# Kernel tuning notes

Hardware: AMD Instinct MI355X
Metric: run time of the kernel (lower is better)

## Reference

```python
import jax, jax.numpy as jnp
import numpy as np

B, T, D = 4, 1024, 1024       # batch, tokens, emb_size
E, K, F_EXP = 8, 2, 1024      # num_expert, num_expert_active, expert_size
NUM_BLOCK = 12


def setup_inputs() -> dict:
    key = jax.random.key(0)
    k_x, k_b, k_r, k_1, k_2 = jax.random.split(key, 5)
    x = jax.random.normal(k_x, (B, T, D), dtype=jnp.float32)
    auxfree_bias = jax.random.normal(k_b, (E,), dtype=jnp.float32) * 0.1
    router_w = jax.random.normal(k_r, (E, D), dtype=jnp.float32) * 0.02
    # GroupedLinear weight{i}: [out_features, in_features], applied as x @ W^T
    w1 = jax.random.normal(k_1, (E, F_EXP, D), dtype=jnp.float32) * 0.02
    w2 = jax.random.normal(k_2, (E, D, F_EXP), dtype=jnp.float32) * (0.02 / np.sqrt(2.0 * NUM_BLOCK))
    return {"x": x, "auxfree_bias": auxfree_bias, "router_w": router_w, "w1": w1, "w2": w2}


def reference(x, auxfree_bias, router_w, w1, w2):
    # --- routing: top-k on bias-adjusted DETACHED logits, gather raw logits ---
    logits = jnp.einsum("btd,ed->bte", x, router_w)              # [B,T,E]
    biased = jax.lax.stop_gradient(logits) + auxfree_bias        # bias only affects selection
    _, idx = jax.lax.top_k(biased, K)                            # [B,T,K] int32
    gathered = jnp.take_along_axis(logits, idx, axis=-1)         # [B,T,K]
    probs = jax.nn.softmax(gathered, axis=-1)                    # [B,T,K]

    # combine weights per expert: sum_k probs_k * 1[idx_k == e]  -> [B,T,E]
    combine = jnp.sum(jax.nn.one_hot(idx, E, dtype=x.dtype) * probs[..., None], axis=2)

    # --- experts: out = sum_e combine_e * (gelu(x W1_e^T) W2_e^T) ---
    # (dense per-expert reference for the dispatch -> grouped GEMM -> combine pipeline;
    #  tokens with combine weight 0 contribute nothing, matching the sparse original)
    out = jnp.zeros_like(x)
    for e in range(E):
        h = jax.nn.gelu(jnp.einsum("btd,fd->btf", x, w1[e]), approximate=False)
        out = out + combine[:, :, e:e + 1] * jnp.einsum("btf,df->btd", h, w2[e])
    return out
```

## Files before the change

kernel.cpp:

```cpp
#include <hip/hip_runtime.h>
#include <hip/hip_bf16.h>

#define D_DIM 1024
#define F_DIM 1024
#define NTOK  4096
#define NEXP  8
#define CAP   4096

typedef __attribute__((ext_vector_type(8))) short bf16x8;
typedef __attribute__((ext_vector_type(4))) float f32x4;
typedef __attribute__((ext_vector_type(8))) unsigned short u16x8;

__device__ __forceinline__ unsigned short f2bf(float f) {
    unsigned int u = __float_as_uint(f);
    u = u + 0x7fffu + ((u >> 16) & 1u);
    return (unsigned short)(u >> 16);
}

__device__ __forceinline__ void async_copy16(void* lds, const void* gsrc) {
    __builtin_amdgcn_global_load_lds(
        (const __attribute__((address_space(1))) unsigned int*)gsrc,
        (__attribute__((address_space(3))) unsigned int*)lds, 16, 0, 0);
}

__global__ __launch_bounds__(256) void cvt_kernel(const float* __restrict__ in,
                                                  unsigned short* __restrict__ out, int n) {
    int i = (blockIdx.x * 256 + threadIdx.x) * 8;
    if (i >= n) return;
    const float4* p = (const float4*)(in + i);
    float4 a = p[0], b = p[1];
    u16x8 r;
    r[0] = f2bf(a.x); r[1] = f2bf(a.y); r[2] = f2bf(a.z); r[3] = f2bf(a.w);
    r[4] = f2bf(b.x); r[5] = f2bf(b.y); r[6] = f2bf(b.z); r[7] = f2bf(b.w);
    *(u16x8*)(out + i) = r;
}

__global__ __launch_bounds__(256) void logits_kernel(
    const float* __restrict__ x, const float* __restrict__ rw,
    float* __restrict__ logits)
{
    const int wave = threadIdx.x >> 6, lane = threadIdx.x & 63;
    const int t = blockIdx.x * 4 + wave;
    double s[NEXP];
    #pragma unroll
    for (int e = 0; e < NEXP; ++e) s[e] = 0.0;
    const float* xp = x + (size_t)t * D_DIM;
    for (int kk = 0; kk < D_DIM; kk += 64) {
        float xv = xp[kk + lane];
        #pragma unroll
        for (int e = 0; e < NEXP; ++e)
            s[e] += (double)xv * (double)rw[e * D_DIM + kk + lane];
    }
    #pragma unroll
    for (int e = 0; e < NEXP; ++e) {
        double v = s[e];
        for (int off = 32; off; off >>= 1) v += __shfl_xor(v, off, 64);
        s[e] = v;
    }
    if (lane == 0) {
        #pragma unroll
        for (int e = 0; e < NEXP; ++e) logits[(size_t)t * NEXP + e] = (float)s[e];
    }
}

__global__ __launch_bounds__(256) void assign_kernel(
    const float* __restrict__ logits, const float* __restrict__ bias,
    int* counts, int* list, float* wlist)
{
    __shared__ int lcnt[NEXP];
    __shared__ int lbase[NEXP];
    const int tid = threadIdx.x;
    const int t = blockIdx.x * 256 + tid;
    if (tid < NEXP) lcnt[tid] = 0;
    __syncthreads();

    float lg[NEXP], b2[NEXP];
    #pragma unroll
    for (int e = 0; e < NEXP; ++e) {
        lg[e] = logits[(size_t)t * NEXP + e];
        b2[e] = lg[e] + bias[e];
    }
    int i0 = 0; float b0v = b2[0], l0v = lg[0];
    #pragma unroll
    for (int e = 1; e < NEXP; ++e)
        if (b2[e] > b0v) { b0v = b2[e]; l0v = lg[e]; i0 = e; }
    int i1 = -1; float b1v = 0.f, l1v = 0.f;
    #pragma unroll
    for (int e = 0; e < NEXP; ++e) {
        if (e == i0) continue;
        bool take = (i1 < 0) || (b2[e] > b1v);
        if (take) { i1 = e; b1v = b2[e]; l1v = lg[e]; }
    }
    float m = fmaxf(l0v, l1v);
    float e0 = expf(l0v - m), e1 = expf(l1v - m);
    float inv = 1.0f / (e0 + e1);

    int lp0 = atomicAdd(&lcnt[i0], 1);
    int lp1 = atomicAdd(&lcnt[i1], 1);
    __syncthreads();
    if (tid < NEXP) lbase[tid] = atomicAdd(&counts[tid], lcnt[tid]);
    __syncthreads();

    int p0 = lbase[i0] + lp0;
    list[i0 * CAP + p0] = t; wlist[i0 * CAP + p0] = e0 * inv;
    int p1 = lbase[i1] + lp1;
    list[i1 * CAP + p1] = t; wlist[i1 * CAP + p1] = e1 * inv;
}

#define STAGE(AB, BB, k0)                                                   \
    do {                                                                    \
        _Pragma("unroll")                                                   \
        for (int i = 0; i < 4; ++i)                                         \
            async_copy16(&AB[(wave * 4 + i) * 512], ap[i] + (k0));          \
        _Pragma("unroll")                                                   \
        for (int i = 0; i < 2; ++i)                                         \
            async_copy16(&BB[(wave * 2 + i) * 512], bp_[i] + (k0));         \
    } while (0)

#define COMPUTE(AB, BB)                                                     \
    do {                                                                    \
        _Pragma("unroll")                                                   \
        for (int kk = 0; kk < 2; ++kk) {                                    \
            bf16x8 af[4], bfv[2];                                           \
            const int phys = (((kk * 4) + (lane >> 4)) ^ (lane & 7)) * 8;   \
            _Pragma("unroll")                                               \
            for (int m = 0; m < 4; ++m)                                     \
                af[m] = *(const bf16x8*)&AB[(wr * 64 + m * 16 + (lane & 15)) * 64 + phys]; \
            _Pragma("unroll")                                               \
            for (int n = 0; n < 2; ++n)                                     \
                bfv[n] = *(const bf16x8*)&BB[(wc * 32 + n * 16 + (lane & 15)) * 64 + phys]; \
            _Pragma("unroll")                                               \
            for (int m = 0; m < 4; ++m)                                     \
                _Pragma("unroll")                                           \
                for (int n = 0; n < 2; ++n)                                 \
                    acc[m][n] = __builtin_amdgcn_mfma_f32_16x16x32_bf16(af[m], bfv[n], acc[m][n], 0, 0, 0); \
        }                                                                   \
    } while (0)

__global__ __launch_bounds__(256) void gemm1_kernel(
    const unsigned short* __restrict__ xb,
    const unsigned short* __restrict__ w1b,
    const int* __restrict__ counts,
    const int* __restrict__ list,
    unsigned short* __restrict__ H)
{
    const int e  = blockIdx.y >> 5;
    const int rb = blockIdx.y & 31;
    const int ne = counts[e];
    if (rb * 128 >= ne) return;
    const int row0 = rb * 128;
    const int n0 = blockIdx.x * 64;
    int hbase = 0;
    #pragma unroll
    for (int ee = 0; ee < NEXP; ++ee) if (ee < e) hbase += counts[ee];

    __shared__ __align__(16) unsigned short As[128 * 64];
    __shared__ __align__(16) unsigned short Bs[64 * 64];
    __shared__ int toks[128];

    const int tid = threadIdx.x;
    if (tid < 128) {
        int i = row0 + tid;
        if (i >= ne) i = ne - 1;
        toks[tid] = list[e * CAP + i];
    }
    __syncthreads();

    const int wave = tid >> 6, lane = tid & 63;
    const int wr = wave >> 1, wc = wave & 1;

    const int lr  = lane >> 3;
    const int swz = ((lane & 7) ^ lr) * 8;
    const unsigned short* ap[4];
    const unsigned short* bp_[2];
    const unsigned short* wbase = w1b + (size_t)e * F_DIM * D_DIM;
    #pragma unroll
    for (int i = 0; i < 4; ++i)
        ap[i] = xb + (size_t)toks[wave * 32 + i * 8 + lr] * D_DIM + swz;
    #pragma unroll
    for (int i = 0; i < 2; ++i)
        bp_[i] = wbase + (size_t)(n0 + wave * 16 + i * 8 + lr) * D_DIM + swz;

    f32x4 acc[4][2];
    #pragma unroll
    for (int m = 0; m < 4; ++m)
        #pragma unroll
        for (int n = 0; n < 2; ++n) acc[m][n] = (f32x4){0.f, 0.f, 0.f, 0.f};

    for (int k0 = 0; k0 < D_DIM; k0 += 64) {
        STAGE(As, Bs, k0);
        __syncthreads();
        COMPUTE(As, Bs);
        __syncthreads();
    }

    #pragma unroll
    for (int m = 0; m < 4; ++m) {
        #pragma unroll
        for (int j = 0; j < 4; ++j) {
            int ri = wr * 64 + m * 16 + (lane >> 4) * 4 + j;
            int i = row0 + ri;
            if (i < ne) {
                unsigned short* hp = H + (size_t)(hbase + i) * F_DIM + n0 + wc * 32;
                #pragma unroll
                for (int n = 0; n < 2; ++n) {
                    float v = acc[m][n][j];
                    float g = 0.5f * v * (1.0f + erff(v * 0.70710678118654752f));
                    hp[n * 16 + (lane & 15)] = f2bf(g);
                }
            }
        }
    }
}

__global__ __launch_bounds__(256) void gemm2_kernel(
    const unsigned short* __restrict__ H,
    const unsigned short* __restrict__ w2b,
    const int* __restrict__ counts,
    const int* __restrict__ list, const float* __restrict__ wlist,
    float* __restrict__ out)
{
    const int e  = blockIdx.y >> 5;
    const int rb = blockIdx.y & 31;
    const int ne = counts[e];
    if (rb * 128 >= ne) return;
    const int row0 = rb * 128;
    const int n0 = blockIdx.x * 64;
    int hbase = 0;
    #pragma unroll
    for (int ee = 0; ee < NEXP; ++ee) if (ee < e) hbase += counts[ee];

    __shared__ __align__(16) unsigned short As[128 * 64];
    __shared__ __align__(16) unsigned short Bs[64 * 64];
    __shared__ int toks[128];
    __shared__ float wts[128];

    const int tid = threadIdx.x;
    if (tid < 128) {
        int i = row0 + tid;
        if (i >= ne) i = ne - 1;
        toks[tid] = list[e * CAP + i];
        wts[tid]  = wlist[e * CAP + i];
    }
    __syncthreads();

    const int wave = tid >> 6, lane = tid & 63;
    const int wr = wave >> 1, wc = wave & 1;

    const int lr  = lane >> 3;
    const int swz = ((lane & 7) ^ lr) * 8;
    const unsigned short* ap[4];
    const unsigned short* bp_[2];
    const unsigned short* wbase = w2b + (size_t)e * D_DIM * F_DIM;
    #pragma unroll
    for (int i = 0; i < 4; ++i)
        ap[i] = H + (size_t)(hbase + row0 + wave * 32 + i * 8 + lr) * F_DIM + swz;
    #pragma unroll
    for (int i = 0; i < 2; ++i)
        bp_[i] = wbase + (size_t)(n0 + wave * 16 + i * 8 + lr) * F_DIM + swz;

    f32x4 acc[4][2];
    #pragma unroll
    for (int m = 0; m < 4; ++m)
        #pragma unroll
        for (int n = 0; n < 2; ++n) acc[m][n] = (f32x4){0.f, 0.f, 0.f, 0.f};

    for (int k0 = 0; k0 < F_DIM; k0 += 64) {
        STAGE(As, Bs, k0);
        __syncthreads();
        COMPUTE(As, Bs);
        __syncthreads();
    }

    #pragma unroll
    for (int m = 0; m < 4; ++m) {
        #pragma unroll
        for (int j = 0; j < 4; ++j) {
            int ri = wr * 64 + m * 16 + (lane >> 4) * 4 + j;
            int i = row0 + ri;
            if (i < ne) {
                int t = toks[ri];
                float wt = wts[ri];
                float* op = out + (size_t)t * D_DIM + n0 + wc * 32;
                #pragma unroll
                for (int n = 0; n < 2; ++n)
                    atomicAdd(&op[n * 16 + (lane & 15)], wt * acc[m][n][j]);
            }
        }
    }
}

extern "C" void kernel_launch(void* const* d_in, const int* in_sizes, int n_in,
                              void* d_out, int out_size, void* d_ws, size_t ws_size,
                              hipStream_t stream)
{
    const float* x    = (const float*)d_in[0];
    const float* bias = (const float*)d_in[1];
    const float* rw   = (const float*)d_in[2];
    const float* w1   = (const float*)d_in[3];
    const float* w2   = (const float*)d_in[4];
    float* out = (float*)d_out;

    char* ws = (char*)d_ws;
    size_t cur = 0;
    auto alloc = [&](size_t bytes) -> void* {
        void* p = (void*)(ws + cur);
        cur += (bytes + 255) & ~(size_t)255;
        return p;
    };
    unsigned short* xb   = (unsigned short*)alloc((size_t)NTOK * D_DIM * 2);
    unsigned short* w1b  = (unsigned short*)alloc((size_t)NEXP * F_DIM * D_DIM * 2);
    unsigned short* w2b  = (unsigned short*)alloc((size_t)NEXP * F_DIM * D_DIM * 2);
    unsigned short* Hb   = (unsigned short*)alloc((size_t)(NTOK * 2 + 128) * F_DIM * 2);
    float* logits = (float*)alloc((size_t)NTOK * NEXP * 4);
    int*   list   = (int*)alloc(NEXP * CAP * 4);
    float* wlist  = (float*)alloc(NEXP * CAP * 4);
    int*   counts = (int*)alloc(64);

    hipMemsetAsync(counts, 0, 64, stream);
    hipMemsetAsync(out, 0, (size_t)out_size * 4, stream);

    cvt_kernel<<<NTOK * D_DIM / 2048, 256, 0, stream>>>(x, xb, NTOK * D_DIM);
    cvt_kernel<<<NEXP * F_DIM * D_DIM / 2048, 256, 0, stream>>>(w1, w1b, NEXP * F_DIM * D_DIM);
    cvt_kernel<<<NEXP * F_DIM * D_DIM / 2048, 256, 0, stream>>>(w2, w2b, NEXP * F_DIM * D_DIM);
    logits_kernel<<<NTOK / 4, 256, 0, stream>>>(x, rw, logits);
    assign_kernel<<<NTOK / 256, 256, 0, stream>>>(logits, bias, counts, list, wlist);
    gemm1_kernel<<<dim3(16, 256), 256, 0, stream>>>(xb, w1b, counts, list, Hb);
    gemm2_kernel<<<dim3(16, 256), 256, 0, stream>>>(Hb, w2b, counts, list, wlist, out);
}
```

Before: 236.5 us.

## Replace atomic scatter-add with expert-ordered output buffer and gather combine kernel

gemm2 now writes unweighted per-expert rows contiguously into an fp32 O2 buffer instead of doing weighted atomicAdd into the output. A new combine kernel gathers each token's two expert rows and applies the softmax weights, so the output memset is no longer needed. The three fp32-to-bf16 conversion launches are merged into a single kernel, and the workspace is laid out by hand with O2 aliasing the xb/w1b region. This trades atomic traffic for an extra 32 MB write plus read, and it depends on correct buffer aliasing across launches.

```diff
diff --git a/kernel.cpp b/kernel.cpp
--- a/kernel.cpp
+++ b/kernel.cpp
@@ -6,6 +6,8 @@
 #define NTOK  4096
 #define NEXP  8
 #define CAP   4096
+#define NGRP_X (NTOK * D_DIM / 8)
+#define NGRP_W (NEXP * F_DIM * D_DIM / 8)
 
 typedef __attribute__((ext_vector_type(8))) short bf16x8;
 typedef __attribute__((ext_vector_type(4))) float f32x4;
@@ -23,16 +25,23 @@
         (__attribute__((address_space(3))) unsigned int*)lds, 16, 0, 0);
 }
 
-__global__ __launch_bounds__(256) void cvt_kernel(const float* __restrict__ in,
-                                                  unsigned short* __restrict__ out, int n) {
-    int i = (blockIdx.x * 256 + threadIdx.x) * 8;
-    if (i >= n) return;
-    const float4* p = (const float4*)(in + i);
+__global__ __launch_bounds__(256) void cvt3_kernel(
+    const float* __restrict__ x, const float* __restrict__ w1, const float* __restrict__ w2,
+    unsigned short* __restrict__ xb, unsigned short* __restrict__ w1b,
+    unsigned short* __restrict__ w2b)
+{
+    long g = (long)blockIdx.x * 256 + threadIdx.x;
+    const float* src; unsigned short* dst; long o;
+    if (g < NGRP_X)            { src = x;  dst = xb;  o = g; }
+    else if (g < NGRP_X + NGRP_W) { src = w1; dst = w1b; o = g - NGRP_X; }
+    else                       { src = w2; dst = w2b; o = g - NGRP_X - NGRP_W; }
+    size_t i = (size_t)o * 8;
+    const float4* p = (const float4*)(src + i);
     float4 a = p[0], b = p[1];
     u16x8 r;
     r[0] = f2bf(a.x); r[1] = f2bf(a.y); r[2] = f2bf(a.z); r[3] = f2bf(a.w);
     r[4] = f2bf(b.x); r[5] = f2bf(b.y); r[6] = f2bf(b.z); r[7] = f2bf(b.w);
-    *(u16x8*)(out + i) = r;
+    *(u16x8*)(dst + i) = r;
 }
 
 __global__ __launch_bounds__(256) void logits_kernel(
@@ -65,7 +74,7 @@
 
 __global__ __launch_bounds__(256) void assign_kernel(
     const float* __restrict__ logits, const float* __restrict__ bias,
-    int* counts, int* list, float* wlist)
+    int* counts, int* list, int* pairEP, float* pairW)
 {
     __shared__ int lcnt[NEXP];
     __shared__ int lbase[NEXP];
@@ -102,9 +111,13 @@
     __syncthreads();
 
     int p0 = lbase[i0] + lp0;
-    list[i0 * CAP + p0] = t; wlist[i0 * CAP + p0] = e0 * inv;
     int p1 = lbase[i1] + lp1;
-    list[i1 * CAP + p1] = t; wlist[i1 * CAP + p1] = e1 * inv;
+    list[i0 * CAP + p0] = t;
+    list[i1 * CAP + p1] = t;
+    pairEP[2 * t]     = (p0 << 3) | i0;
+    pairEP[2 * t + 1] = (p1 << 3) | i1;
+    pairW[2 * t]      = e0 * inv;
+    pairW[2 * t + 1]  = e1 * inv;
 }
 
 #define STAGE(AB, BB, k0)                                                   \
@@ -217,8 +230,7 @@
     const unsigned short* __restrict__ H,
     const unsigned short* __restrict__ w2b,
     const int* __restrict__ counts,
-    const int* __restrict__ list, const float* __restrict__ wlist,
-    float* __restrict__ out)
+    float* __restrict__ O2)
 {
     const int e  = blockIdx.y >> 5;
     const int rb = blockIdx.y & 31;
@@ -232,18 +244,8 @@
 
     __shared__ __align__(16) unsigned short As[128 * 64];
     __shared__ __align__(16) unsigned short Bs[64 * 64];
-    __shared__ int toks[128];
-    __shared__ float wts[128];
 
     const int tid = threadIdx.x;
-    if (tid < 128) {
-        int i = row0 + tid;
-        if (i >= ne) i = ne - 1;
-        toks[tid] = list[e * CAP + i];
-        wts[tid]  = wlist[e * CAP + i];
-    }
-    __syncthreads();
-
     const int wave = tid >> 6, lane = tid & 63;
     const int wr = wave >> 1, wc = wave & 1;
 
@@ -279,15 +281,44 @@
             int ri = wr * 64 + m * 16 + (lane >> 4) * 4 + j;
             int i = row0 + ri;
             if (i < ne) {
-                int t = toks[ri];
-                float wt = wts[ri];
-                float* op = out + (size_t)t * D_DIM + n0 + wc * 32;
+                float* op = O2 + (size_t)(hbase + i) * D_DIM + n0 + wc * 32;
                 #pragma unroll
                 for (int n = 0; n < 2; ++n)
-                    atomicAdd(&op[n * 16 + (lane & 15)], wt * acc[m][n][j]);
+                    op[n * 16 + (lane & 15)] = acc[m][n][j];
             }
         }
     }
+}
+
+__global__ __launch_bounds__(256) void combine_kernel(
+    const float* __restrict__ O2, const int* __restrict__ counts,
+    const int* __restrict__ pairEP, const float* __restrict__ pairW,
+    float* __restrict__ out)
+{
+    const int t = blockIdx.x;
+    const int tid = threadIdx.x;
+    int offs[NEXP];
+    int a = 0;
+    #pragma unroll
+    for (int e = 0; e < NEXP; ++e) { offs[e] = a; a += counts[e]; }
+    int ep0 = pairEP[2 * t], ep1 = pairEP[2 * t + 1];
+    float w0 = pairW[2 * t], w1 = pairW[2 * t + 1];
+    int e0 = ep0 & 7, e1 = ep1 & 7, o0 = 0, o1 = 0;
+    #pragma unroll
+    for (int e = 0; e < NEXP; ++e) {
+        if (e == e0) o0 = offs[e];
+        if (e == e1) o1 = offs[e];
+    }
+    size_t r0 = (size_t)(o0 + (ep0 >> 3)) * D_DIM;
+    size_t r1 = (size_t)(o1 + (ep1 >> 3)) * D_DIM;
+    float4 va = *(const float4*)(O2 + r0 + tid * 4);
+    float4 vb = *(const float4*)(O2 + r1 + tid * 4);
+    float4 r;
+    r.x = w0 * va.x + w1 * vb.x;
+    r.y = w0 * va.y + w1 * vb.y;
+    r.z = w0 * va.z + w1 * vb.z;
+    r.w = w0 * va.w + w1 * vb.w;
+    *(float4*)(out + (size_t)t * D_DIM + tid * 4) = r;
 }
 
 extern "C" void kernel_launch(void* const* d_in, const int* in_sizes, int n_in,
@@ -302,29 +333,24 @@
     float* out = (float*)d_out;
 
     char* ws = (char*)d_ws;
-    size_t cur = 0;
-    auto alloc = [&](size_t bytes) -> void* {
-        void* p = (void*)(ws + cur);
-        cur += (bytes + 255) & ~(size_t)255;
-        return p;
-    };
-    unsigned short* xb   = (unsigned short*)alloc((size_t)NTOK * D_DIM * 2);
-    unsigned short* w1b  = (unsigned short*)alloc((size_t)NEXP * F_DIM * D_DIM * 2);
-    unsigned short* w2b  = (unsigned short*)alloc((size_t)NEXP * F_DIM * D_DIM * 2);
-    unsigned short* Hb   = (unsigned short*)alloc((size_t)(NTOK * 2 + 128) * F_DIM * 2);
-    float* logits = (float*)alloc((size_t)NTOK * NEXP * 4);
-    int*   list   = (int*)alloc(NEXP * CAP * 4);
-    float* wlist  = (float*)alloc(NEXP * CAP * 4);
-    int*   counts = (int*)alloc(64);
+    unsigned short* w2b = (unsigned short*)(ws);
+    unsigned short* Hb  = (unsigned short*)(ws + 16777216);
+    float*          O2  = (float*)        (ws + 33816576);
+    unsigned short* xb  = (unsigned short*)(ws + 33816576);
+    unsigned short* w1b = (unsigned short*)(ws + 33816576 + 8388608);
+    char* tail = ws + 33816576 + 34078720;
+    float* logits = (float*)(tail);
+    int*   list   = (int*)(tail + 131072);
+    int*   pairEP = (int*)(tail + 262144);
+    float* pairW  = (float*)(tail + 294912);
+    int*   counts = (int*)(tail + 327680);
 
     hipMemsetAsync(counts, 0, 64, stream);
-    hipMemsetAsync(out, 0, (size_t)out_size * 4, stream);
-
-    cvt_kernel<<<NTOK * D_DIM / 2048, 256, 0, stream>>>(x, xb, NTOK * D_DIM);
-    cvt_kernel<<<NEXP * F_DIM * D_DIM / 2048, 256, 0, stream>>>(w1, w1b, NEXP * F_DIM * D_DIM);
-    cvt_kernel<<<NEXP * F_DIM * D_DIM / 2048, 256, 0, stream>>>(w2, w2b, NEXP * F_DIM * D_DIM);
+
+    cvt3_kernel<<<(NGRP_X + 2 * NGRP_W) / 256, 256, 0, stream>>>(x, w1, w2, xb, w1b, w2b);
     logits_kernel<<<NTOK / 4, 256, 0, stream>>>(x, rw, logits);
-    assign_kernel<<<NTOK / 256, 256, 0, stream>>>(logits, bias, counts, list, wlist);
+    assign_kernel<<<NTOK / 256, 256, 0, stream>>>(logits, bias, counts, list, pairEP, pairW);
     gemm1_kernel<<<dim3(16, 256), 256, 0, stream>>>(xb, w1b, counts, list, Hb);
-    gemm2_kernel<<<dim3(16, 256), 256, 0, stream>>>(Hb, w2b, counts, list, wlist, out);
-}
+    gemm2_kernel<<<dim3(16, 256), 256, 0, stream>>>(Hb, w2b, counts, O2);
+    combine_kernel<<<NTOK, 256, 0, stream>>>(O2, counts, pairEP, pairW, out);
+}
```

Result: faster. 218.9 us (-7.4%).
